# Performance work log

Hardware: AMD Instinct MI355X
Metric: run time of the kernel (lower is better)

Reference implementation:

```python
import jax, jax.numpy as jnp
import numpy as np

N_NODES = 40000
N_EDGES = 640000
D = 128


def setup_inputs() -> dict:
    key = jax.random.key(0)
    ks = jax.random.split(key, 7)
    x = jax.random.normal(ks[0], (N_NODES, D), dtype=jnp.float32)
    edge_index = jax.random.randint(ks[1], (2, N_EDGES), 0, N_NODES, dtype=jnp.int64)
    # uniform in [0.5, 1.5) to avoid division blow-up near zero
    edge_attr = jax.random.uniform(ks[2], (N_EDGES,), dtype=jnp.float32) + 0.5
    s = 1.0 / np.sqrt(D)
    W1 = jax.random.uniform(ks[3], (D, D), dtype=jnp.float32, minval=-s, maxval=s)
    b1 = jax.random.uniform(ks[4], (D,), dtype=jnp.float32, minval=-s, maxval=s)
    W2 = jax.random.uniform(ks[5], (D, D), dtype=jnp.float32, minval=-s, maxval=s)
    b2 = jax.random.uniform(ks[6], (D,), dtype=jnp.float32, minval=-s, maxval=s)
    return {"x": x, "edge_index": edge_index, "edge_attr": edge_attr,
            "W1": W1, "b1": b1, "W2": W2, "b2": b2}


def _layer(x, src, dst, edge_attr, W, b, num_nodes):
    # message: gather source features, divide by per-edge scalar
    msg = x[src] / edge_attr[:, None]                      # [E, D]
    # aggregate: scatter-add into destination nodes
    agg = jax.ops.segment_sum(msg, dst, num_segments=num_nodes)  # [N, D]
    # linear (torch: y = x @ W.T + b) then leaky_relu(0.01)
    y = agg @ W.T + b
    return jnp.where(y >= 0, y, 0.01 * y)


def reference(x, edge_index, edge_attr, W1, b1, W2, b2):
    src, dst = edge_index[0], edge_index[1]
    n = x.shape[0]
    x = jnp.maximum(_layer(x, src, dst, edge_attr, W1, b1, n), 0.0)
    x = jnp.maximum(_layer(x, src, dst, edge_attr, W2, b2, n), 0.0)
    return x
```

## Files before the change

### kernel.cpp

```cpp
#include <hip/hip_runtime.h>

#define D 128
#define CAP 64
typedef unsigned short u16;
typedef unsigned int   u32;

typedef __attribute__((ext_vector_type(8))) short short8;
typedef __attribute__((ext_vector_type(4))) float f32x4;

__device__ __forceinline__ u32 f2bf(float f) {
    u32 u = __float_as_uint(f);
    u += 0x7fffu + ((u >> 16) & 1u);
    return u >> 16;
}
__device__ __forceinline__ float2 bf2x2(u32 u) {
    float2 r;
    r.x = __uint_as_float(u << 16);
    r.y = __uint_as_float(u & 0xffff0000u);
    return r;
}

__global__ __launch_bounds__(256) void prep_kernel(
    const float4* __restrict__ x, uint2* __restrict__ xb,
    const float4* __restrict__ W1, const float4* __restrict__ W2,
    uint2* __restrict__ wb1, uint2* __restrict__ wb2,
    const int* __restrict__ src, const int* __restrict__ dst,
    const float* __restrict__ attr, int* __restrict__ counts,
    u32* __restrict__ combo, int E, int n4, int cvtb, int Nper, int N)
{
    const int bid = blockIdx.x;
    const int t   = threadIdx.x;

    if (bid < cvtb) {
        int i = bid * 256 + t;
        if (i < n4) {
            float4 v = x[i];
            uint2 o;
            o.x = f2bf(v.x) | (f2bf(v.y) << 16);
            o.y = f2bf(v.z) | (f2bf(v.w) << 16);
            xb[i] = o;
        }
    } else if (bid < cvtb + 32) {
        int i = (bid - cvtb) * 256 + t;
        const float4* in = (i < 4096) ? W1 : W2;
        uint2* out = (i < 4096) ? wb1 : wb2;
        int k = i & 4095;
        float4 v = in[k];
        uint2 o;
        o.x = f2bf(v.x) | (f2bf(v.y) << 16);
        o.y = f2bf(v.z) | (f2bf(v.w) << 16);
        out[k] = o;
    } else {
        const int sb    = bid - cvtb - 32;
        const int xcd   = sb & 7;
        const int chunk = sb >> 3;
        const int lo    = xcd * Nper;
        const int hi    = min(lo + Nper, N);
        long long e0 = (long long)chunk * 1024 + t * 4;

        if (e0 + 3 < E) {
            int4   s4 = *(const int4*)(src + e0);
            int4   d4 = *(const int4*)(dst + e0);
            float4 a4 = *(const float4*)(attr + e0);
            #pragma unroll
            for (int q = 0; q < 4; ++q) {
                int d = (q == 0) ? d4.x : (q == 1) ? d4.y : (q == 2) ? d4.z : d4.w;
                if (d >= lo && d < hi) {
                    int s = (q == 0) ? s4.x : (q == 1) ? s4.y : (q == 2) ? s4.z : s4.w;
                    float a = (q == 0) ? a4.x : (q == 1) ? a4.y : (q == 2) ? a4.z : a4.w;
                    int r = atomicAdd(&counts[d], 1);
                    if (r < CAP)
                        combo[((long long)d << 6) + r] =
                            (u32)s | (f2bf(1.0f / a) << 16);
                }
            }
        } else {
            for (int q = 0; q < 4; ++q) {
                long long e = e0 + q;
                if (e < E) {
                    int d = dst[e];
                    if (d >= lo && d < hi) {
                        int r = atomicAdd(&counts[d], 1);
                        if (r < CAP)
                            combo[((long long)d << 6) + r] =
                                (u32)src[e] | (f2bf(1.0f / attr[e]) << 16);
                    }
                }
            }
        }
    }
}

template <bool OUT_BF16>
__global__ __launch_bounds__(512) void fused_layer_kernel(
    const u16* __restrict__ X, const u32* __restrict__ combo,
    const int* __restrict__ counts, const u16* __restrict__ Wb,
    const float* __restrict__ bias, void* __restrict__ Yv, int Nper, int N)
{
    __shared__ u16 As[32 * D];

    const int w    = threadIdx.x >> 6;
    const int lane = threadIdx.x & 63;
    const int g    = lane >> 4;
    const int c16  = lane & 15;

    const int xcd   = blockIdx.x & 7;
    const int slice = blockIdx.x >> 3;
    const int nl0   = slice * 32 + w * 4;
    const int nbase = xcd * Nper;

    int cnt4[4]; u32 ce4[4];
    #pragma unroll
    for (int i = 0; i < 4; ++i) {
        int nl = nl0 + i;
        bool v = (nl < Nper) && (nbase + nl < N);
        cnt4[i] = v ? min(counts[nbase + nl], CAP) : 0;
        ce4[i]  = v ? combo[((long long)(nbase + nl) << 6) + lane] : 0u;
    }

    #pragma unroll
    for (int i = 0; i < 4; ++i) {
        const int cnt = cnt4[i];
        const u32 ce  = ce4[i];
        float acc[8];
        #pragma unroll
        for (int c = 0; c < 8; ++c) acc[c] = 0.f;

        int j = 0;
        for (; j + 7 < cnt; j += 8) {
            u32 e0 = __shfl(ce, j + g);
            u32 e1 = __shfl(ce, j + 4 + g);
            uint4 r0 = *(const uint4*)(X + (long long)(e0 & 0xffffu) * D + c16 * 8);
            uint4 r1 = *(const uint4*)(X + (long long)(e1 & 0xffffu) * D + c16 * 8);
            float f0 = __uint_as_float(e0 & 0xffff0000u);
            float f1 = __uint_as_float(e1 & 0xffff0000u);
            float2 v;
            v = bf2x2(r0.x); acc[0] += v.x * f0; acc[1] += v.y * f0;
            v = bf2x2(r0.y); acc[2] += v.x * f0; acc[3] += v.y * f0;
            v = bf2x2(r0.z); acc[4] += v.x * f0; acc[5] += v.y * f0;
            v = bf2x2(r0.w); acc[6] += v.x * f0; acc[7] += v.y * f0;
            v = bf2x2(r1.x); acc[0] += v.x * f1; acc[1] += v.y * f1;
            v = bf2x2(r1.y); acc[2] += v.x * f1; acc[3] += v.y * f1;
            v = bf2x2(r1.z); acc[4] += v.x * f1; acc[5] += v.y * f1;
            v = bf2x2(r1.w); acc[6] += v.x * f1; acc[7] += v.y * f1;
        }
        for (; j + 3 < cnt; j += 4) {
            u32 e0 = __shfl(ce, j + g);
            uint4 r0 = *(const uint4*)(X + (long long)(e0 & 0xffffu) * D + c16 * 8);
            float f0 = __uint_as_float(e0 & 0xffff0000u);
            float2 v;
            v = bf2x2(r0.x); acc[0] += v.x * f0; acc[1] += v.y * f0;
            v = bf2x2(r0.y); acc[2] += v.x * f0; acc[3] += v.y * f0;
            v = bf2x2(r0.z); acc[4] += v.x * f0; acc[5] += v.y * f0;
            v = bf2x2(r0.w); acc[6] += v.x * f0; acc[7] += v.y * f0;
        }
        {
            int rem = cnt - j;
            u32 e0 = __shfl(ce, j + g);
            if (g < rem) {
                uint4 r0 = *(const uint4*)(X + (long long)(e0 & 0xffffu) * D + c16 * 8);
                float f0 = __uint_as_float(e0 & 0xffff0000u);
                float2 v;
                v = bf2x2(r0.x); acc[0] += v.x * f0; acc[1] += v.y * f0;
                v = bf2x2(r0.y); acc[2] += v.x * f0; acc[3] += v.y * f0;
                v = bf2x2(r0.z); acc[4] += v.x * f0; acc[5] += v.y * f0;
                v = bf2x2(r0.w); acc[6] += v.x * f0; acc[7] += v.y * f0;
            }
        }

        #pragma unroll
        for (int c = 0; c < 8; ++c) {
            acc[c] += __shfl_xor(acc[c], 16);
            acc[c] += __shfl_xor(acc[c], 32);
        }

        if (g == 0) {
            uint4 o;
            o.x = f2bf(acc[0]) | (f2bf(acc[1]) << 16);
            o.y = f2bf(acc[2]) | (f2bf(acc[3]) << 16);
            o.z = f2bf(acc[4]) | (f2bf(acc[5]) << 16);
            o.w = f2bf(acc[6]) | (f2bf(acc[7]) << 16);
            int row  = w * 4 + i;
            int slot = c16 ^ (row & 7);
            *(uint4*)&As[row * D + slot * 8] = o;
        }
    }

    __syncthreads();

    const int mrow = lane & 15;
    const int kq   = lane >> 4;
    const int h    = w >> 2;
    const int q    = w & 3;
    const int lr0  = h * 16;

    short8 afr[4];
    const u16* asrc = As + (lr0 + mrow) * D;
    #pragma unroll
    for (int ks = 0; ks < 4; ++ks)
        afr[ks] = *(const short8*)(asrc + ((kq + ks * 4) ^ (mrow & 7)) * 8);

    #pragma unroll
    for (int jn = 0; jn < 2; ++jn) {
        const int n0 = q * 32 + jn * 16;
        float bv = bias[n0 + mrow];
        f32x4 acc = {bv, bv, bv, bv};
        const u16* wrow = Wb + (long long)(n0 + mrow) * D + kq * 8;
        #pragma unroll
        for (int ks = 0; ks < 4; ++ks) {
            short8 bfr = *(const short8*)(wrow + ks * 32);
            acc = __builtin_amdgcn_mfma_f32_16x16x32_bf16(afr[ks], bfr, acc, 0, 0, 0);
        }
        #pragma unroll
        for (int r = 0; r < 4; ++r) {
            float v = acc[r] > 0.f ? acc[r] : 0.f;
            int lrow = lr0 + kq * 4 + r;
            int nl   = slice * 32 + lrow;
            if (nl < Nper && nbase + nl < N) {
                long long off = (long long)(nbase + nl) * D + n0 + mrow;
                if (OUT_BF16)
                    *((u16*)Yv + off) = (u16)f2bf(v);
                else
                    *((float*)Yv + off) = v;
            }
        }
    }
}

extern "C" void kernel_launch(void* const* d_in, const int* in_sizes, int n_in,
                              void* d_out, int out_size, void* d_ws, size_t ws_size,
                              hipStream_t stream)
{
    const float* x    = (const float*)d_in[0];
    const int*   eidx = (const int*)d_in[1];
    const float* attr = (const float*)d_in[2];
    const float* W1   = (const float*)d_in[3];
    const float* b1   = (const float*)d_in[4];
    const float* W2   = (const float*)d_in[5];
    const float* b2   = (const float*)d_in[6];

    const int N = in_sizes[0] / D;
    const int E = in_sizes[2];
    const int* src = eidx;
    const int* dst = eidx + E;
    const int Nper = (N + 7) / 8;

    char* p = (char*)d_ws;
    u16*  xb    = (u16*)p;   p += ((size_t)N * D * 2 + 15) & ~15ULL;
    u16*  aggB  = (u16*)p;   p += ((size_t)N * D * 2 + 15) & ~15ULL;
    u32*  combo = (u32*)p;   p += (size_t)N * CAP * 4;
    u16*  wb1   = (u16*)p;   p += (size_t)D * D * 2;
    u16*  wb2   = (u16*)p;   p += (size_t)D * D * 2;
    int*  counts= (int*)p;

    const int n4    = N * D / 4;
    const int cvtb  = (n4 + 255) / 256;
    const int hfb   = 8 * ((E + 1023) / 1024);
    const int prepb = cvtb + 32 + hfb;
    const int fusedb = 8 * ((Nper + 31) / 32);

    hipMemsetAsync(counts, 0, (size_t)N * 4, stream);
    prep_kernel<<<prepb, 256, 0, stream>>>(
        (const float4*)x, (uint2*)xb, (const float4*)W1, (const float4*)W2,
        (uint2*)wb1, (uint2*)wb2, src, dst, attr, counts,
        combo, E, n4, cvtb, Nper, N);

    fused_layer_kernel<true><<<fusedb, 512, 0, stream>>>(
        xb, combo, counts, wb1, b1, aggB, Nper, N);
    fused_layer_kernel<false><<<fusedb, 512, 0, stream>>>(
        aggB, combo, counts, wb2, b2, d_out, Nper, N);
}
```

Measured before the change: 185.1 us.

## Merge prep and both layers into one persistent kernel with grid barriers

Replaces the three kernel launches (prep plus two fused layers) with a single persistent kernel of 512 blocks. Phases are separated by atomic grid-wide barriers, and the layer and edge-bucketing work is spread over the blocks with grid-stride loops. The goal is to remove launch gaps and tail effects between kernels. In exchange it depends on all 512 blocks being co-resident (launch bounds of 4 blocks per CU), and blocks spin-wait at each barrier.

```diff
diff --git a/kernel.cpp b/kernel.cpp
--- a/kernel.cpp
+++ b/kernel.cpp
@@ -20,144 +20,90 @@
     return r;
 }
 
-__global__ __launch_bounds__(256) void prep_kernel(
-    const float4* __restrict__ x, uint2* __restrict__ xb,
-    const float4* __restrict__ W1, const float4* __restrict__ W2,
-    uint2* __restrict__ wb1, uint2* __restrict__ wb2,
-    const int* __restrict__ src, const int* __restrict__ dst,
-    const float* __restrict__ attr, int* __restrict__ counts,
-    u32* __restrict__ combo, int E, int n4, int cvtb, int Nper, int N)
+struct KParams {
+    const float4* x;      uint2* xb;
+    const float4* W1;     const float4* W2;
+    uint2* wb1;           uint2* wb2;
+    const int* src;       const int* dst;    const float* attr;
+    int* counts;          u32* combo;
+    u16* aggB;
+    const float* b1;      const float* b2;
+    float* out;
+    int* bar;
+    int E, n4, Nper, N, nBlocks;
+};
+
+__device__ __forceinline__ void grid_barrier(int* slot, int nBlocks)
 {
-    const int bid = blockIdx.x;
-    const int t   = threadIdx.x;
-
-    if (bid < cvtb) {
-        int i = bid * 256 + t;
-        if (i < n4) {
-            float4 v = x[i];
-            uint2 o;
-            o.x = f2bf(v.x) | (f2bf(v.y) << 16);
-            o.y = f2bf(v.z) | (f2bf(v.w) << 16);
-            xb[i] = o;
-        }
-    } else if (bid < cvtb + 32) {
-        int i = (bid - cvtb) * 256 + t;
-        const float4* in = (i < 4096) ? W1 : W2;
-        uint2* out = (i < 4096) ? wb1 : wb2;
-        int k = i & 4095;
-        float4 v = in[k];
-        uint2 o;
-        o.x = f2bf(v.x) | (f2bf(v.y) << 16);
-        o.y = f2bf(v.z) | (f2bf(v.w) << 16);
-        out[k] = o;
-    } else {
-        const int sb    = bid - cvtb - 32;
-        const int xcd   = sb & 7;
-        const int chunk = sb >> 3;
-        const int lo    = xcd * Nper;
-        const int hi    = min(lo + Nper, N);
-        long long e0 = (long long)chunk * 1024 + t * 4;
-
-        if (e0 + 3 < E) {
-            int4   s4 = *(const int4*)(src + e0);
-            int4   d4 = *(const int4*)(dst + e0);
-            float4 a4 = *(const float4*)(attr + e0);
-            #pragma unroll
-            for (int q = 0; q < 4; ++q) {
-                int d = (q == 0) ? d4.x : (q == 1) ? d4.y : (q == 2) ? d4.z : d4.w;
-                if (d >= lo && d < hi) {
-                    int s = (q == 0) ? s4.x : (q == 1) ? s4.y : (q == 2) ? s4.z : s4.w;
-                    float a = (q == 0) ? a4.x : (q == 1) ? a4.y : (q == 2) ? a4.z : a4.w;
-                    int r = atomicAdd(&counts[d], 1);
-                    if (r < CAP)
-                        combo[((long long)d << 6) + r] =
-                            (u32)s | (f2bf(1.0f / a) << 16);
-                }
-            }
-        } else {
-            for (int q = 0; q < 4; ++q) {
-                long long e = e0 + q;
-                if (e < E) {
-                    int d = dst[e];
-                    if (d >= lo && d < hi) {
-                        int r = atomicAdd(&counts[d], 1);
-                        if (r < CAP)
-                            combo[((long long)d << 6) + r] =
-                                (u32)src[e] | (f2bf(1.0f / attr[e]) << 16);
-                    }
-                }
-            }
-        }
-    }
+    __syncthreads();
+    if (threadIdx.x == 0) {
+        __threadfence();
+        __hip_atomic_fetch_add(slot, 1, __ATOMIC_ACQ_REL, __HIP_MEMORY_SCOPE_AGENT);
+        while (__hip_atomic_load(slot, __ATOMIC_ACQUIRE, __HIP_MEMORY_SCOPE_AGENT)
+               < nBlocks)
+            __builtin_amdgcn_s_sleep(8);
+        __threadfence();
+    }
+    __syncthreads();
 }
 
 template <bool OUT_BF16>
-__global__ __launch_bounds__(512) void fused_layer_kernel(
-    const u16* __restrict__ X, const u32* __restrict__ combo,
-    const int* __restrict__ counts, const u16* __restrict__ Wb,
-    const float* __restrict__ bias, void* __restrict__ Yv, int Nper, int N)
+__device__ __forceinline__ void layer_phase(
+    u16* __restrict__ As, const u16* __restrict__ X,
+    const u32* __restrict__ combo, const int* __restrict__ counts,
+    const u16* __restrict__ Wb, const float* __restrict__ bias,
+    void* __restrict__ Yv, int Nper, int N)
 {
-    __shared__ u16 As[32 * D];
-
-    const int w    = threadIdx.x >> 6;
-    const int lane = threadIdx.x & 63;
+    const int tid  = threadIdx.x;
+    const int w    = tid >> 6;
+    const int lane = tid & 63;
     const int g    = lane >> 4;
     const int c16  = lane & 15;
-
-    const int xcd   = blockIdx.x & 7;
-    const int slice = blockIdx.x >> 3;
-    const int nl0   = slice * 32 + w * 4;
-    const int nbase = xcd * Nper;
-
-    int cnt4[4]; u32 ce4[4];
-    #pragma unroll
-    for (int i = 0; i < 4; ++i) {
-        int nl = nl0 + i;
-        bool v = (nl < Nper) && (nbase + nl < N);
-        cnt4[i] = v ? min(counts[nbase + nl], CAP) : 0;
-        ce4[i]  = v ? combo[((long long)(nbase + nl) << 6) + lane] : 0u;
-    }
-
-    #pragma unroll
-    for (int i = 0; i < 4; ++i) {
-        const int cnt = cnt4[i];
-        const u32 ce  = ce4[i];
-        float acc[8];
+    const int nTiles = 8 * ((Nper + 31) / 32);
+
+    for (int vt = blockIdx.x; vt < nTiles; vt += gridDim.x) {
+        const int xcd   = vt & 7;
+        const int slice = vt >> 3;
+        const int nl0   = slice * 32 + w * 4;
+        const int nbase = xcd * Nper;
+
+        int cnt4[4]; u32 ce4[4];
         #pragma unroll
-        for (int c = 0; c < 8; ++c) acc[c] = 0.f;
-
-        int j = 0;
-        for (; j + 7 < cnt; j += 8) {
-            u32 e0 = __shfl(ce, j + g);
-            u32 e1 = __shfl(ce, j + 4 + g);
-            uint4 r0 = *(const uint4*)(X + (long long)(e0 & 0xffffu) * D + c16 * 8);
-            uint4 r1 = *(const uint4*)(X + (long long)(e1 & 0xffffu) * D + c16 * 8);
-            float f0 = __uint_as_float(e0 & 0xffff0000u);
-            float f1 = __uint_as_float(e1 & 0xffff0000u);
-            float2 v;
-            v = bf2x2(r0.x); acc[0] += v.x * f0; acc[1] += v.y * f0;
-            v = bf2x2(r0.y); acc[2] += v.x * f0; acc[3] += v.y * f0;
-            v = bf2x2(r0.z); acc[4] += v.x * f0; acc[5] += v.y * f0;
-            v = bf2x2(r0.w); acc[6] += v.x * f0; acc[7] += v.y * f0;
-            v = bf2x2(r1.x); acc[0] += v.x * f1; acc[1] += v.y * f1;
-            v = bf2x2(r1.y); acc[2] += v.x * f1; acc[3] += v.y * f1;
-            v = bf2x2(r1.z); acc[4] += v.x * f1; acc[5] += v.y * f1;
-            v = bf2x2(r1.w); acc[6] += v.x * f1; acc[7] += v.y * f1;
+        for (int i = 0; i < 4; ++i) {
+            int nl = nl0 + i;
+            bool v = (nl < Nper) && (nbase + nl < N);
+            cnt4[i] = v ? min(counts[nbase + nl], CAP) : 0;
+            ce4[i]  = v ? combo[((long long)(nbase + nl) << 6) + lane] : 0u;
         }
-        for (; j + 3 < cnt; j += 4) {
-            u32 e0 = __shfl(ce, j + g);
-            uint4 r0 = *(const uint4*)(X + (long long)(e0 & 0xffffu) * D + c16 * 8);
-            float f0 = __uint_as_float(e0 & 0xffff0000u);
-            float2 v;
-            v = bf2x2(r0.x); acc[0] += v.x * f0; acc[1] += v.y * f0;
-            v = bf2x2(r0.y); acc[2] += v.x * f0; acc[3] += v.y * f0;
-            v = bf2x2(r0.z); acc[4] += v.x * f0; acc[5] += v.y * f0;
-            v = bf2x2(r0.w); acc[6] += v.x * f0; acc[7] += v.y * f0;
-        }
-        {
-            int rem = cnt - j;
-            u32 e0 = __shfl(ce, j + g);
-            if (g < rem) {
+
+        #pragma unroll
+        for (int i = 0; i < 4; ++i) {
+            const int cnt = cnt4[i];
+            const u32 ce  = ce4[i];
+            float acc[8];
+            #pragma unroll
+            for (int c = 0; c < 8; ++c) acc[c] = 0.f;
+
+            int j = 0;
+            for (; j + 7 < cnt; j += 8) {
+                u32 e0 = __shfl(ce, j + g);
+                u32 e1 = __shfl(ce, j + 4 + g);
+                uint4 r0 = *(const uint4*)(X + (long long)(e0 & 0xffffu) * D + c16 * 8);
+                uint4 r1 = *(const uint4*)(X + (long long)(e1 & 0xffffu) * D + c16 * 8);
+                float f0 = __uint_as_float(e0 & 0xffff0000u);
+                float f1 = __uint_as_float(e1 & 0xffff0000u);
+                float2 v;
+                v = bf2x2(r0.x); acc[0] += v.x * f0; acc[1] += v.y * f0;
+                v = bf2x2(r0.y); acc[2] += v.x * f0; acc[3] += v.y * f0;
+                v = bf2x2(r0.z); acc[4] += v.x * f0; acc[5] += v.y * f0;
+                v = bf2x2(r0.w); acc[6] += v.x * f0; acc[7] += v.y * f0;
+                v = bf2x2(r1.x); acc[0] += v.x * f1; acc[1] += v.y * f1;
+                v = bf2x2(r1.y); acc[2] += v.x * f1; acc[3] += v.y * f1;
+                v = bf2x2(r1.z); acc[4] += v.x * f1; acc[5] += v.y * f1;
+                v = bf2x2(r1.w); acc[6] += v.x * f1; acc[7] += v.y * f1;
+            }
+            for (; j + 3 < cnt; j += 4) {
+                u32 e0 = __shfl(ce, j + g);
                 uint4 r0 = *(const uint4*)(X + (long long)(e0 & 0xffffu) * D + c16 * 8);
                 float f0 = __uint_as_float(e0 & 0xffff0000u);
                 float2 v;
@@ -166,65 +112,157 @@
                 v = bf2x2(r0.z); acc[4] += v.x * f0; acc[5] += v.y * f0;
                 v = bf2x2(r0.w); acc[6] += v.x * f0; acc[7] += v.y * f0;
             }
+            {
+                int rem = cnt - j;
+                u32 e0 = __shfl(ce, j + g);
+                if (g < rem) {
+                    uint4 r0 = *(const uint4*)(X + (long long)(e0 & 0xffffu) * D + c16 * 8);
+                    float f0 = __uint_as_float(e0 & 0xffff0000u);
+                    float2 v;
+                    v = bf2x2(r0.x); acc[0] += v.x * f0; acc[1] += v.y * f0;
+                    v = bf2x2(r0.y); acc[2] += v.x * f0; acc[3] += v.y * f0;
+                    v = bf2x2(r0.z); acc[4] += v.x * f0; acc[5] += v.y * f0;
+                    v = bf2x2(r0.w); acc[6] += v.x * f0; acc[7] += v.y * f0;
+                }
+            }
+
+            #pragma unroll
+            for (int c = 0; c < 8; ++c) {
+                acc[c] += __shfl_xor(acc[c], 16);
+                acc[c] += __shfl_xor(acc[c], 32);
+            }
+
+            if (g == 0) {
+                uint4 o;
+                o.x = f2bf(acc[0]) | (f2bf(acc[1]) << 16);
+                o.y = f2bf(acc[2]) | (f2bf(acc[3]) << 16);
+                o.z = f2bf(acc[4]) | (f2bf(acc[5]) << 16);
+                o.w = f2bf(acc[6]) | (f2bf(acc[7]) << 16);
+                int rowi = w * 4 + i;
+                int slot = c16 ^ (rowi & 7);
+                *(uint4*)&As[rowi * D + slot * 8] = o;
+            }
         }
 
+        __syncthreads();
+
+        const int mrow = lane & 15;
+        const int kq   = lane >> 4;
+        const int h    = w >> 2;
+        const int q    = w & 3;
+        const int lr0  = h * 16;
+
+        short8 afr[4];
+        const u16* asrc = As + (lr0 + mrow) * D;
         #pragma unroll
-        for (int c = 0; c < 8; ++c) {
-            acc[c] += __shfl_xor(acc[c], 16);
-            acc[c] += __shfl_xor(acc[c], 32);
+        for (int ks = 0; ks < 4; ++ks)
+            afr[ks] = *(const short8*)(asrc + ((kq + ks * 4) ^ (mrow & 7)) * 8);
+
+        #pragma unroll
+        for (int jn = 0; jn < 2; ++jn) {
+            const int n0 = q * 32 + jn * 16;
+            float bv = bias[n0 + mrow];
+            f32x4 acc2 = {bv, bv, bv, bv};
+            const u16* wrow = Wb + (long long)(n0 + mrow) * D + kq * 8;
+            #pragma unroll
+            for (int ks = 0; ks < 4; ++ks) {
+                short8 bfr = *(const short8*)(wrow + ks * 32);
+                acc2 = __builtin_amdgcn_mfma_f32_16x16x32_bf16(afr[ks], bfr, acc2, 0, 0, 0);
+            }
+            #pragma unroll
+            for (int r = 0; r < 4; ++r) {
+                float v = acc2[r] > 0.f ? acc2[r] : 0.f;
+                int lrow = lr0 + kq * 4 + r;
+                int nl   = slice * 32 + lrow;
+                if (nl < Nper && nbase + nl < N) {
+                    long long off = (long long)(nbase + nl) * D + n0 + mrow;
+                    if (OUT_BF16)
+                        *((u16*)Yv + off) = (u16)f2bf(v);
+                    else
+                        *((float*)Yv + off) = v;
+                }
+            }
         }
 
-        if (g == 0) {
-            uint4 o;
-            o.x = f2bf(acc[0]) | (f2bf(acc[1]) << 16);
-            o.y = f2bf(acc[2]) | (f2bf(acc[3]) << 16);
-            o.z = f2bf(acc[4]) | (f2bf(acc[5]) << 16);
-            o.w = f2bf(acc[6]) | (f2bf(acc[7]) << 16);
-            int row  = w * 4 + i;
-            int slot = c16 ^ (row & 7);
-            *(uint4*)&As[row * D + slot * 8] = o;
+        __syncthreads();
+    }
+}
+
+__global__ __launch_bounds__(512, 4) void mega_kernel(KParams P)
+{
+    __shared__ u16 As[32 * D];
+
+    const int tid = threadIdx.x;
+    const int gsz = gridDim.x * 512;
+    const int gt  = blockIdx.x * 512 + tid;
+
+    for (int i = gt; i < P.n4; i += gsz) {
+        float4 v = P.x[i];
+        uint2 o;
+        o.x = f2bf(v.x) | (f2bf(v.y) << 16);
+        o.y = f2bf(v.z) | (f2bf(v.w) << 16);
+        P.xb[i] = o;
+    }
+    for (int i = gt; i < 8192; i += gsz) {
+        const float4* in = (i < 4096) ? P.W1 : P.W2;
+        uint2* outw = (i < 4096) ? P.wb1 : P.wb2;
+        int k = i & 4095;
+        float4 v = in[k];
+        uint2 o;
+        o.x = f2bf(v.x) | (f2bf(v.y) << 16);
+        o.y = f2bf(v.z) | (f2bf(v.w) << 16);
+        outw[k] = o;
+    }
+
+    {
+        const int nchunks = (P.E + 2047) / 2048;
+        for (int sb = blockIdx.x; sb < 8 * nchunks; sb += gridDim.x) {
+            const int xcd   = sb & 7;
+            const int chunk = sb >> 3;
+            const int lo    = xcd * P.Nper;
+            const int hi    = min(lo + P.Nper, P.N);
+            long long e0 = (long long)chunk * 2048 + tid * 4;
+
+            if (e0 + 3 < P.E) {
+                int4   s4 = *(const int4*)(P.src + e0);
+                int4   d4 = *(const int4*)(P.dst + e0);
+                float4 a4 = *(const float4*)(P.attr + e0);
+                #pragma unroll
+                for (int q = 0; q < 4; ++q) {
+                    int d = (q == 0) ? d4.x : (q == 1) ? d4.y : (q == 2) ? d4.z : d4.w;
+                    if (d >= lo && d < hi) {
+                        int s = (q == 0) ? s4.x : (q == 1) ? s4.y : (q == 2) ? s4.z : s4.w;
+                        float a = (q == 0) ? a4.x : (q == 1) ? a4.y : (q == 2) ? a4.z : a4.w;
+                        int r = atomicAdd(&P.counts[d], 1);
+                        if (r < CAP)
+                            P.combo[((long long)d << 6) + r] =
+                                (u32)s | (f2bf(1.0f / a) << 16);
+                    }
+                }
+            } else {
+                for (int q = 0; q < 4; ++q) {
+                    long long e = e0 + q;
+                    if (e < P.E) {
+                        int d = P.dst[e];
+                        if (d >= lo && d < hi) {
+                            int r = atomicAdd(&P.counts[d], 1);
+                            if (r < CAP)
+                                P.combo[((long long)d << 6) + r] =
+                                    (u32)P.src[e] | (f2bf(1.0f / P.attr[e]) << 16);
+                        }
+                    }
+                }
+            }
         }
     }
-
-    __syncthreads();
-
-    const int mrow = lane & 15;
-    const int kq   = lane >> 4;
-    const int h    = w >> 2;
-    const int q    = w & 3;
-    const int lr0  = h * 16;
-
-    short8 afr[4];
-    const u16* asrc = As + (lr0 + mrow) * D;
-    #pragma unroll
-    for (int ks = 0; ks < 4; ++ks)
-        afr[ks] = *(const short8*)(asrc + ((kq + ks * 4) ^ (mrow & 7)) * 8);
-
-    #pragma unroll
-    for (int jn = 0; jn < 2; ++jn) {
-        const int n0 = q * 32 + jn * 16;
-        float bv = bias[n0 + mrow];
-        f32x4 acc = {bv, bv, bv, bv};
-        const u16* wrow = Wb + (long long)(n0 + mrow) * D + kq * 8;
-        #pragma unroll
-        for (int ks = 0; ks < 4; ++ks) {
-            short8 bfr = *(const short8*)(wrow + ks * 32);
-            acc = __builtin_amdgcn_mfma_f32_16x16x32_bf16(afr[ks], bfr, acc, 0, 0, 0);
-        }
-        #pragma unroll
-        for (int r = 0; r < 4; ++r) {
-            float v = acc[r] > 0.f ? acc[r] : 0.f;
-            int lrow = lr0 + kq * 4 + r;
-            int nl   = slice * 32 + lrow;
-            if (nl < Nper && nbase + nl < N) {
-                long long off = (long long)(nbase + nl) * D + n0 + mrow;
-                if (OUT_BF16)
-                    *((u16*)Yv + off) = (u16)f2bf(v);
-                else
-                    *((float*)Yv + off) = v;
-            }
-        }
-    }
+    grid_barrier(&P.bar[0], P.nBlocks);
+
+    layer_phase<true>(As, (const u16*)P.xb, P.combo, P.counts,
+                      (const u16*)P.wb1, P.b1, P.aggB, P.Nper, P.N);
+    grid_barrier(&P.bar[1], P.nBlocks);
+
+    layer_phase<false>(As, P.aggB, P.combo, P.counts,
+                       (const u16*)P.wb2, P.b2, P.out, P.Nper, P.N);
 }
 
 extern "C" void kernel_launch(void* const* d_in, const int* in_sizes, int n_in,
@@ -241,8 +279,6 @@
 
     const int N = in_sizes[0] / D;
     const int E = in_sizes[2];
-    const int* src = eidx;
-    const int* dst = eidx + E;
     const int Nper = (N + 7) / 8;
 
     char* p = (char*)d_ws;
@@ -251,22 +287,22 @@
     u32*  combo = (u32*)p;   p += (size_t)N * CAP * 4;
     u16*  wb1   = (u16*)p;   p += (size_t)D * D * 2;
     u16*  wb2   = (u16*)p;   p += (size_t)D * D * 2;
-    int*  counts= (int*)p;
-
-    const int n4    = N * D / 4;
-    const int cvtb  = (n4 + 255) / 256;
-    const int hfb   = 8 * ((E + 1023) / 1024);
-    const int prepb = cvtb + 32 + hfb;
-    const int fusedb = 8 * ((Nper + 31) / 32);
-
-    hipMemsetAsync(counts, 0, (size_t)N * 4, stream);
-    prep_kernel<<<prepb, 256, 0, stream>>>(
-        (const float4*)x, (uint2*)xb, (const float4*)W1, (const float4*)W2,
-        (uint2*)wb1, (uint2*)wb2, src, dst, attr, counts,
-        combo, E, n4, cvtb, Nper, N);
-
-    fused_layer_kernel<true><<<fusedb, 512, 0, stream>>>(
-        xb, combo, counts, wb1, b1, aggB, Nper, N);
-    fused_layer_kernel<false><<<fusedb, 512, 0, stream>>>(
-        aggB, combo, counts, wb2, b2, d_out, Nper, N);
-}
+    int*  counts= (int*)p;   p += (size_t)N * 4;
+    int*  bar   = (int*)p;
+
+    KParams P;
+    P.x = (const float4*)x;  P.xb = (uint2*)xb;
+    P.W1 = (const float4*)W1; P.W2 = (const float4*)W2;
+    P.wb1 = (uint2*)wb1;     P.wb2 = (uint2*)wb2;
+    P.src = eidx;            P.dst = eidx + E;     P.attr = attr;
+    P.counts = counts;       P.combo = combo;
+    P.aggB = aggB;
+    P.b1 = b1;               P.b2 = b2;
+    P.out = (float*)d_out;
+    P.bar = bar;
+    P.E = E;  P.n4 = N * D / 4;  P.Nper = Nper;  P.N = N;
+    P.nBlocks = 512;
+
+    hipMemsetAsync(counts, 0, (size_t)N * 4 + 16, stream);
+    mega_kernel<<<512, 512, 0, stream>>>(P);
+}
```

After: 363.3 us. 96.3% more time.
